# Kernel tuning notes

Measured on AMD Instinct MI355X. Metric: run time of the kernel, lower is better.

The kernel has to match this reference:

```python
import jax, jax.numpy as jnp
import numpy as np

B, T, L, H = 512, 512, 64, 512  # batch, time_steps, sequence_len, hidden_dim


def gru_cell(x, h, W_ih, W_hh, b_ih, b_hh):
    # PyTorch GRUCell math. W_ih: [3H, in], W_hh: [3H, H]; gate order (r, z, n).
    gi = x @ W_ih.T + b_ih
    gh = h @ W_hh.T + b_hh
    i_r, i_z, i_n = jnp.split(gi, 3, axis=-1)
    h_r, h_z, h_n = jnp.split(gh, 3, axis=-1)
    r = jax.nn.sigmoid(i_r + h_r)
    z = jax.nn.sigmoid(i_z + h_z)
    n = jnp.tanh(i_n + r * h_n)
    return (1.0 - z) * n + z * h


def setup_inputs() -> dict:
    key = jax.random.key(0)
    ks = jax.random.split(key, 12)
    s = 1.0 / np.sqrt(H)  # PyTorch GRUCell/Linear init scale
    u = lambda k, shape: jax.random.uniform(k, shape, jnp.float32, -s, s)
    return {
        "x": jax.random.normal(ks[0], (B, T + L - 1), jnp.float32),
        "h_1": jnp.zeros((B, H), jnp.float32),
        "h_2": jnp.zeros((B, H), jnp.float32),
        "W_ih1": u(ks[1], (3 * H, T)),
        "W_hh1": u(ks[2], (3 * H, H)),
        "b_ih1": u(ks[3], (3 * H,)),
        "b_hh1": u(ks[4], (3 * H,)),
        "W_ih2": u(ks[5], (3 * H, H)),
        "W_hh2": u(ks[6], (3 * H, H)),
        "b_ih2": u(ks[7], (3 * H,)),
        "b_hh2": u(ks[8], (3 * H,)),
        "W_fc": u(ks[9], (1, H)),
        "b_fc": u(ks[10], (1,)),
    }


def reference(x, h_1, h_2, W_ih1, W_hh1, b_ih1, b_hh1,
              W_ih2, W_hh2, b_ih2, b_hh2, W_fc, b_fc):
    # Sliding windows x[:, t:t+T] for t in [0, L): gather once, scan over steps.
    idx = jnp.arange(L)[:, None] + jnp.arange(T)[None, :]  # [L, T]
    xs = jnp.transpose(x[:, idx], (1, 0, 2))  # [L, B, T]

    def step(carry, x_t):
        h1, h2 = carry
        h1 = gru_cell(x_t, h1, W_ih1, W_hh1, b_ih1, b_hh1)
        h2 = gru_cell(h1, h2, W_ih2, W_hh2, b_ih2, b_hh2)
        y = (h2 @ W_fc.T + b_fc)[:, 0]  # [B]
        return (h1, h2), y

    (h1, h2), ys = jax.lax.scan(step, (h_1, h_2), xs)
    return ys.T, h1, h2  # output_seq [B, L], final hidden states
```

## Files before the change

### kernel.cpp

```cpp
#include <hip/hip_runtime.h>
#include <hip/hip_bf16.h>
#include <math.h>

typedef __attribute__((ext_vector_type(8))) short short8;
typedef __attribute__((ext_vector_type(4))) float f32x4;
typedef unsigned short u16;
typedef unsigned int u32;

__device__ __forceinline__ u16 f2bf(float f) {
  union { float f; u32 u; } x; x.f = f;
  return (u16)((x.u + 0x7fffu + ((x.u >> 16) & 1u)) >> 16);
}
__device__ __forceinline__ float sigm(float v) {
  return __builtin_amdgcn_rcpf(1.0f + __expf(-v));
}
__device__ __forceinline__ float tanh_fast(float v) {
  return 1.0f - 2.0f * __builtin_amdgcn_rcpf(1.0f + __expf(2.0f * v));
}

#define MFMA __builtin_amdgcn_mfma_f32_16x16x32_bf16
#define HS 262144

#define LDG16_BODY(FL)                                        \
    "global_load_dwordx4 %0, %16, off " FL "\n\t"             \
    "global_load_dwordx4 %1, %16, off offset:64 " FL "\n\t"   \
    "global_load_dwordx4 %2, %16, off offset:128 " FL "\n\t"  \
    "global_load_dwordx4 %3, %16, off offset:192 " FL "\n\t"  \
    "global_load_dwordx4 %4, %16, off offset:256 " FL "\n\t"  \
    "global_load_dwordx4 %5, %16, off offset:320 " FL "\n\t"  \
    "global_load_dwordx4 %6, %16, off offset:384 " FL "\n\t"  \
    "global_load_dwordx4 %7, %16, off offset:448 " FL "\n\t"  \
    "global_load_dwordx4 %8, %16, off offset:512 " FL "\n\t"  \
    "global_load_dwordx4 %9, %16, off offset:576 " FL "\n\t"  \
    "global_load_dwordx4 %10, %16, off offset:640 " FL "\n\t" \
    "global_load_dwordx4 %11, %16, off offset:704 " FL "\n\t" \
    "global_load_dwordx4 %12, %16, off offset:768 " FL "\n\t" \
    "global_load_dwordx4 %13, %16, off offset:832 " FL "\n\t" \
    "global_load_dwordx4 %14, %16, off offset:896 " FL "\n\t" \
    "global_load_dwordx4 %15, %16, off offset:960 " FL
#define LDG16_OPS(a, base)                                                     \
    : "=&v"(a[0]), "=&v"(a[1]), "=&v"(a[2]), "=&v"(a[3]), "=&v"(a[4]),         \
      "=&v"(a[5]), "=&v"(a[6]), "=&v"(a[7]), "=&v"(a[8]), "=&v"(a[9]),         \
      "=&v"(a[10]), "=&v"(a[11]), "=&v"(a[12]), "=&v"(a[13]), "=&v"(a[14]),    \
      "=&v"(a[15])                                                             \
    : "v"(base) : "memory"

__device__ __forceinline__ void ldg16nw_sc0(short8 a[16], const u16* base) {
  asm volatile(LDG16_BODY("sc0") LDG16_OPS(a, base));
}
__device__ __forceinline__ void ldg16nw_sc01(short8 a[16], const u16* base) {
  asm volatile(LDG16_BODY("sc0 sc1") LDG16_OPS(a, base));
}
#define VMCNT16() do { asm volatile("s_waitcnt vmcnt(16)" ::: "memory"); \
                       __builtin_amdgcn_sched_barrier(0); } while (0)
#define VMCNT0()  do { asm volatile("s_waitcnt vmcnt(0)"  ::: "memory"); \
                       __builtin_amdgcn_sched_barrier(0); } while (0)

__device__ __forceinline__ void stg_sc01(u32* p, u32 v) {
  asm volatile("global_store_dword %0, %1, off sc0 sc1" :: "v"(p), "v"(v) : "memory");
}

__device__ __forceinline__ void waits_nf(unsigned* a, unsigned ta, unsigned* b, unsigned tb) {
  if (threadIdx.x == 0) {
    while (__hip_atomic_load(a, __ATOMIC_RELAXED, __HIP_MEMORY_SCOPE_AGENT) < ta)
      __builtin_amdgcn_s_sleep(1);
    while (__hip_atomic_load(b, __ATOMIC_RELAXED, __HIP_MEMORY_SCOPE_AGENT) < tb)
      __builtin_amdgcn_s_sleep(1);
  }
  __syncthreads();
}

__device__ __forceinline__ float ydot(const short8 a[16], const float* wfcl, int quad) {
  float y = 0.0f;
  #pragma unroll
  for (int s = 0; s < 16; ++s) {
    const float4 wa = *(const float4*)&wfcl[32 * s + quad * 8];
    const float4 wb = *(const float4*)&wfcl[32 * s + quad * 8 + 4];
    union { short8 v; u32 u4[4]; } aa; aa.v = a[s];
    #pragma unroll
    for (int k = 0; k < 4; ++k) {
      union { u32 u; float f; } lo, hi;
      lo.u = aa.u4[k] << 16;
      hi.u = aa.u4[k] & 0xffff0000u;
      float w0 = (k < 2) ? ((k & 1) ? wa.z : wa.x) : ((k & 1) ? wb.z : wb.x);
      float w1 = (k < 2) ? ((k & 1) ? wa.w : wa.y) : ((k & 1) ? wb.w : wb.y);
      y = fmaf(lo.f, w0, y);
      y = fmaf(hi.f, w1, y);
    }
  }
  return y;
}

__global__ __launch_bounds__(256, 1) void gru_fused(
    const float* __restrict__ xin, const float* __restrict__ h1in, const float* __restrict__ h2in,
    const float* __restrict__ Wih1, const float* __restrict__ Whh1,
    const float* __restrict__ bih1, const float* __restrict__ bhh1,
    const float* __restrict__ Wih2, const float* __restrict__ Whh2,
    const float* __restrict__ bih2, const float* __restrict__ bhh2,
    const float* __restrict__ Wfc, const float* __restrict__ bfc,
    float* __restrict__ out, u16* __restrict__ wsb, unsigned* __restrict__ barc)
{
  const int bid   = blockIdx.x;
  const int rb    = bid & 3;
  const int layer = (bid >> 2) & 1;
  const int cbl   = bid >> 3;
  const int n0    = cbl * 16;
  const int wid   = bid >> 2;
  const int tid   = threadIdx.x;
  const int w     = tid >> 6;
  const int lane  = tid & 63;
  const int quad  = lane >> 4;
  const int m16   = lane & 15;

  u16* x0  = wsb;
  u16* x1  = x0 + 512 * 576;
  u16* h1r = x1 + 512 * 576;
  u16* h2r = h1r + 4 * HS;
  u16* h1m = h2r + 4 * HS;

  __shared__ short8 wlds[96 * 64];
  __shared__ float wfcl[512];

  unsigned* c0    = barc + rb * 32;
  unsigned* c1    = barc + 256 + rb * 32;
  unsigned* cinit = barc + 512;

  const float* Wih = layer ? Wih2 : Wih1;
  const float* Whh = layer ? Whh2 : Whh1;
  const float* bih = layer ? bih2 : bih1;
  const float* bhh = layer ? bhh2 : bhh1;

  for (int i = wid * 256 + tid; i < 128 * 575; i += 64 * 256) {
    int r = i / 575, c = i - r * 575;
    int row = rb * 128 + r;
    u16 bv = f2bf(xin[row * 575 + c]);
    x0[row * 576 + c] = bv;
    if (c >= 1) x1[row * 576 + (c - 1)] = bv;
  }
  for (int i = wid * 256 + tid; i < 128 * 512; i += 64 * 256) {
    int r = i >> 9, c = i & 511;
    int row = rb * 128 + r;
    u16 h1v = f2bf(h1in[row * 512 + c]);
    h1r[3 * HS + row * 512 + c] = h1v;
    h2r[3 * HS + row * 512 + c] = f2bf(h2in[row * 512 + c]);
  }
  for (int i = tid; i < 96 * 64; i += 256) {
    int blk = i >> 6, l = i & 63;
    int s, gr;
    if (blk < 64) { s = blk & 31; gr = (blk >> 5) * 512; }
    else          { s = blk - 64; gr = 1024; }
    int n  = n0 + (l & 15);
    int k0 = s * 32 + (l >> 4) * 8;
    short8 pk;
    #pragma unroll
    for (int j = 0; j < 8; ++j) {
      int k = k0 + j;
      float v = (k < 512) ? Wih[(gr + n) * 512 + k] : Whh[(gr + n) * 512 + (k - 512)];
      pk[j] = (short)f2bf(v);
    }
    wlds[blk * 64 + l] = pk;
  }
  for (int i = tid; i < 512; i += 256) wfcl[i] = Wfc[i];

  float hreg[2][4];
  const float* hin = layer ? h2in : h1in;
  #pragma unroll
  for (int rf = 0; rf < 2; ++rf)
    #pragma unroll
    for (int q = 0; q < 4; ++q)
      hreg[rf][q] = hin[(rb * 128 + (2 * w + rf) * 16 + quad * 4 + q) * 512 + n0 + m16];

  const int nn = n0 + m16;
  const float bias_r  = bih[nn] + bhh[nn];
  const float bias_z  = bih[512 + nn] + bhh[512 + nn];
  const float bias_in = bih[1024 + nn];
  const float bias_hn = bhh[1024 + nn];
  const float bfcv = bfc[0];

  __syncthreads();
  if (tid == 0) {
    __builtin_amdgcn_fence(__ATOMIC_RELEASE, "agent");
    __hip_atomic_fetch_add(cinit, 1u, __ATOMIC_RELAXED, __HIP_MEMORY_SCOPE_AGENT);
    while (__hip_atomic_load(cinit, __ATOMIC_RELAXED, __HIP_MEMORY_SCOPE_AGENT) < 256u)
      __builtin_amdgcn_s_sleep(1);
    __builtin_amdgcn_fence(__ATOMIC_ACQUIRE, "agent");
  }
  __syncthreads();

  const int arow0 = rb * 128 + (2 * w) * 16 + m16;
  const int arow1 = arow0 + 16;

  if (layer == 0) {
    for (int u = 0; u < 64; ++u) {
      f32x4 acc[2][4] = {};
      {
        const int c = u & 1;
        const u16* xc = c ? x1 : x0;
        const u32* pa0 = (const u32*)(xc + (size_t)arow0 * 576 + (u - c) + quad * 8);
        const u32* pa1 = (const u32*)(xc + (size_t)arow1 * 576 + (u - c) + quad * 8);
        #pragma unroll
        for (int s = 0; s < 16; ++s) {
          union { short8 v; u32 u4[4]; } a0, a1;
          #pragma unroll
          for (int j = 0; j < 4; ++j) { a0.u4[j] = pa0[s * 16 + j]; a1.u4[j] = pa1[s * 16 + j]; }
          short8 br = wlds[(s)      * 64 + lane];
          short8 bz = wlds[(32 + s) * 64 + lane];
          short8 bi = wlds[(64 + s) * 64 + lane];
          acc[0][0] = MFMA(a0.v, br, acc[0][0], 0, 0, 0);
          acc[1][0] = MFMA(a1.v, br, acc[1][0], 0, 0, 0);
          acc[0][1] = MFMA(a0.v, bz, acc[0][1], 0, 0, 0);
          acc[1][1] = MFMA(a1.v, bz, acc[1][1], 0, 0, 0);
          acc[0][2] = MFMA(a0.v, bi, acc[0][2], 0, 0, 0);
          acc[1][2] = MFMA(a1.v, bi, acc[1][2], 0, 0, 0);
        }
      }
      waits_nf(c0, 32u * (unsigned)u, c1, u >= 4 ? 32u * (unsigned)(u - 3) : 0u);
      {
        short8 a0[16], a1[16];
        const u16* hb = h1r + (size_t)((u + 3) & 3) * HS + quad * 8;
        ldg16nw_sc0(a0, hb + (size_t)arow0 * 512);
        ldg16nw_sc0(a1, hb + (size_t)arow1 * 512);
        VMCNT16();
        #pragma unroll
        for (int s = 0; s < 16; ++s) {
          short8 br = wlds[(16 + s) * 64 + lane];
          short8 bz = wlds[(48 + s) * 64 + lane];
          short8 bh = wlds[(80 + s) * 64 + lane];
          acc[0][0] = MFMA(a0[s], br, acc[0][0], 0, 0, 0);
          acc[0][1] = MFMA(a0[s], bz, acc[0][1], 0, 0, 0);
          acc[0][3] = MFMA(a0[s], bh, acc[0][3], 0, 0, 0);
        }
        VMCNT0();
        #pragma unroll
        for (int s = 0; s < 16; ++s) {
          short8 br = wlds[(16 + s) * 64 + lane];
          short8 bz = wlds[(48 + s) * 64 + lane];
          short8 bh = wlds[(80 + s) * 64 + lane];
          acc[1][0] = MFMA(a1[s], br, acc[1][0], 0, 0, 0);
          acc[1][1] = MFMA(a1[s], bz, acc[1][1], 0, 0, 0);
          acc[1][3] = MFMA(a1[s], bh, acc[1][3], 0, 0, 0);
        }
      }
      {
        u32* hw32 = (u32*)(h1r + (size_t)(u & 3) * HS);
        u32* hm   = (u32*)(h1m + (size_t)(u & 3) * HS);
        #pragma unroll
        for (int rf = 0; rf < 2; ++rf)
          #pragma unroll
          for (int q = 0; q < 4; ++q) {
            float rg = sigm(acc[rf][0][q] + bias_r);
            float zg = sigm(acc[rf][1][q] + bias_z);
            float ng = tanh_fast(acc[rf][2][q] + bias_in + rg * (acc[rf][3][q] + bias_hn));
            float hv = (1.0f - zg) * ng + zg * hreg[rf][q];
            hreg[rf][q] = hv;
            int row = rb * 128 + (2 * w + rf) * 16 + quad * 4 + q;
            u16 b = f2bf(hv);
            int pb = __shfl_xor((int)(u32)b, 1);
            if (!(m16 & 1)) {
              u32 pr = (u32)b | ((u32)(u16)pb << 16);
              int pi = (row * 512 + nn) >> 1;
              hw32[pi] = pr;
              stg_sc01(&hm[pi], pr);
            }
          }
      }
      asm volatile("s_waitcnt vmcnt(0)" ::: "memory");
      __syncthreads();
      if (tid == 0)
        __hip_atomic_fetch_add(c0, 1u, __ATOMIC_RELAXED, __HIP_MEMORY_SCOPE_AGENT);
    }
  } else {
    const bool ywg = (cbl == 0);
    for (int v = 0; v < 64; ++v) {
      f32x4 acc[2][4] = {};
      waits_nf(c1, 32u * (unsigned)v, c0, 32u * (unsigned)(v + 1));
      float ya0 = 0.0f, ya1 = 0.0f;
      {
        short8 a0[16], a1[16];
        const u16* hb = h2r + (size_t)((v + 3) & 3) * HS + quad * 8;
        ldg16nw_sc0(a0, hb + (size_t)arow0 * 512);
        ldg16nw_sc0(a1, hb + (size_t)arow1 * 512);
        VMCNT16();
        #pragma unroll
        for (int s = 0; s < 16; ++s) {
          short8 br = wlds[(16 + s) * 64 + lane];
          short8 bz = wlds[(48 + s) * 64 + lane];
          short8 bh = wlds[(80 + s) * 64 + lane];
          acc[0][0] = MFMA(a0[s], br, acc[0][0], 0, 0, 0);
          acc[0][1] = MFMA(a0[s], bz, acc[0][1], 0, 0, 0);
          acc[0][3] = MFMA(a0[s], bh, acc[0][3], 0, 0, 0);
        }
        if (ywg && v > 0) ya0 = ydot(a0, wfcl, quad);
        VMCNT0();
        #pragma unroll
        for (int s = 0; s < 16; ++s) {
          short8 br = wlds[(16 + s) * 64 + lane];
          short8 bz = wlds[(48 + s) * 64 + lane];
          short8 bh = wlds[(80 + s) * 64 + lane];
          acc[1][0] = MFMA(a1[s], br, acc[1][0], 0, 0, 0);
          acc[1][1] = MFMA(a1[s], bz, acc[1][1], 0, 0, 0);
          acc[1][3] = MFMA(a1[s], bh, acc[1][3], 0, 0, 0);
        }
        if (ywg && v > 0) ya1 = ydot(a1, wfcl, quad);
      }
      {
        short8 b0[16], b1[16];
        const u16* hb = h1m + (size_t)(v & 3) * HS + quad * 8;
        ldg16nw_sc01(b0, hb + (size_t)arow0 * 512);
        ldg16nw_sc01(b1, hb + (size_t)arow1 * 512);
        VMCNT16();
        #pragma unroll
        for (int s = 0; s < 16; ++s) {
          short8 br = wlds[(s)      * 64 + lane];
          short8 bz = wlds[(32 + s) * 64 + lane];
          short8 bi = wlds[(64 + s) * 64 + lane];
          acc[0][0] = MFMA(b0[s], br, acc[0][0], 0, 0, 0);
          acc[0][1] = MFMA(b0[s], bz, acc[0][1], 0, 0, 0);
          acc[0][2] = MFMA(b0[s], bi, acc[0][2], 0, 0, 0);
        }
        VMCNT0();
        #pragma unroll
        for (int s = 0; s < 16; ++s) {
          short8 br = wlds[(s)      * 64 + lane];
          short8 bz = wlds[(32 + s) * 64 + lane];
          short8 bi = wlds[(64 + s) * 64 + lane];
          acc[1][0] = MFMA(b1[s], br, acc[1][0], 0, 0, 0);
          acc[1][1] = MFMA(b1[s], bz, acc[1][1], 0, 0, 0);
          acc[1][2] = MFMA(b1[s], bi, acc[1][2], 0, 0, 0);
        }
      }
      {
        u32* hw32 = (u32*)(h2r + (size_t)(v & 3) * HS);
        #pragma unroll
        for (int rf = 0; rf < 2; ++rf)
          #pragma unroll
          for (int q = 0; q < 4; ++q) {
            float rg = sigm(acc[rf][0][q] + bias_r);
            float zg = sigm(acc[rf][1][q] + bias_z);
            float ng = tanh_fast(acc[rf][2][q] + bias_in + rg * (acc[rf][3][q] + bias_hn));
            float hv = (1.0f - zg) * ng + zg * hreg[rf][q];
            hreg[rf][q] = hv;
            int row = rb * 128 + (2 * w + rf) * 16 + quad * 4 + q;
            u16 b = f2bf(hv);
            int pb = __shfl_xor((int)(u32)b, 1);
            if (!(m16 & 1))
              hw32[(row * 512 + nn) >> 1] = (u32)b | ((u32)(u16)pb << 16);
          }
      }
      asm volatile("s_waitcnt vmcnt(0)" ::: "memory");
      __syncthreads();
      if (tid == 0)
        __hip_atomic_fetch_add(c1, 1u, __ATOMIC_RELAXED, __HIP_MEMORY_SCOPE_AGENT);
      if (ywg && v > 0) {
        ya0 += __shfl_xor(ya0, 16); ya0 += __shfl_xor(ya0, 32);
        ya1 += __shfl_xor(ya1, 16); ya1 += __shfl_xor(ya1, 32);
        if (quad == 0) {
          out[arow0 * 64 + (v - 1)] = ya0 + bfcv;
          out[arow1 * 64 + (v - 1)] = ya1 + bfcv;
        }
      }
    }
    if (ywg) {
      waits_nf(c1, 32u * 64u, c1, 32u * 64u);
      short8 a0[16], a1[16];
      const u16* hb = h2r + (size_t)3 * HS + quad * 8;
      ldg16nw_sc0(a0, hb + (size_t)arow0 * 512);
      ldg16nw_sc0(a1, hb + (size_t)arow1 * 512);
      VMCNT16();
      float ya0 = ydot(a0, wfcl, quad);
      VMCNT0();
      float ya1 = ydot(a1, wfcl, quad);
      ya0 += __shfl_xor(ya0, 16); ya0 += __shfl_xor(ya0, 32);
      ya1 += __shfl_xor(ya1, 16); ya1 += __shfl_xor(ya1, 32);
      if (quad == 0) {
        out[arow0 * 64 + 63] = ya0 + bfcv;
        out[arow1 * 64 + 63] = ya1 + bfcv;
      }
    }
  }

  float* hout = out + 32768 + layer * (512 * 512);
  #pragma unroll
  for (int rf = 0; rf < 2; ++rf)
    #pragma unroll
    for (int q = 0; q < 4; ++q) {
      int row = rb * 128 + (2 * w + rf) * 16 + quad * 4 + q;
      hout[row * 512 + nn] = hreg[rf][q];
    }
}

extern "C" void kernel_launch(void* const* d_in, const int* in_sizes, int n_in,
                              void* d_out, int out_size, void* d_ws, size_t ws_size,
                              hipStream_t stream) {
  (void)in_sizes; (void)n_in; (void)out_size; (void)ws_size;
  hipMemsetAsync(d_out, 0, 32768 * sizeof(float), stream);
  hipMemsetAsync(d_ws, 0, 4096, stream);
  unsigned* bar = (unsigned*)d_ws;
  u16* wsb = (u16*)((char*)d_ws + 4096);
  gru_fused<<<256, 256, 0, stream>>>(
      (const float*)d_in[0], (const float*)d_in[1], (const float*)d_in[2],
      (const float*)d_in[3], (const float*)d_in[4], (const float*)d_in[5], (const float*)d_in[6],
      (const float*)d_in[7], (const float*)d_in[8], (const float*)d_in[9], (const float*)d_in[10],
      (const float*)d_in[11], (const float*)d_in[12],
      (float*)d_out, wsb, bar);
}
```

Baseline: 801.9 us.

## Use eight pre-shifted bf16 x copies for aligned vector loads, shrink h ring buffers

The input sequence is now stored as eight column-shifted bf16 copies. Each sliding-window A operand for layer 0 can then be fetched with aligned 16-byte global_load_dwordx4 instructions instead of many scalar u32 loads. The h1r/h2r recurrence buffers drop from four slots to two, and h1m's slot 3 is seeded with the initial h1. The split VMCNT16/VMCNT0 waits that overlapped the second half of each load with the first half of the MFMAs are replaced by a single full wait, with the MFMAs for both row groups interleaved. This trades a larger prologue copy and less load/compute overlap for fewer, wider loads and a smaller working set.

```diff
diff --git a/kernel.cpp b/kernel.cpp
--- a/kernel.cpp
+++ b/kernel.cpp
@@ -20,6 +20,7 @@
 
 #define MFMA __builtin_amdgcn_mfma_f32_16x16x32_bf16
 #define HS 262144
+#define XS (512*576)
 
 #define LDG16_BODY(FL)                                        \
     "global_load_dwordx4 %0, %16, off " FL "\n\t"             \
@@ -45,15 +46,18 @@
       "=&v"(a[15])                                                             \
     : "v"(base) : "memory"
 
+__device__ __forceinline__ void ldg16nw(short8 a[16], const u16* base) {
+  asm volatile(LDG16_BODY("") LDG16_OPS(a, base));
+}
 __device__ __forceinline__ void ldg16nw_sc0(short8 a[16], const u16* base) {
   asm volatile(LDG16_BODY("sc0") LDG16_OPS(a, base));
 }
 __device__ __forceinline__ void ldg16nw_sc01(short8 a[16], const u16* base) {
   asm volatile(LDG16_BODY("sc0 sc1") LDG16_OPS(a, base));
 }
+#define VMCNT0()  do { asm volatile("s_waitcnt vmcnt(0)"  ::: "memory"); \
+                       __builtin_amdgcn_sched_barrier(0); } while (0)
 #define VMCNT16() do { asm volatile("s_waitcnt vmcnt(16)" ::: "memory"); \
-                       __builtin_amdgcn_sched_barrier(0); } while (0)
-#define VMCNT0()  do { asm volatile("s_waitcnt vmcnt(0)"  ::: "memory"); \
                        __builtin_amdgcn_sched_barrier(0); } while (0)
 
 __device__ __forceinline__ void stg_sc01(u32* p, u32 v) {
@@ -112,11 +116,10 @@
   const int quad  = lane >> 4;
   const int m16   = lane & 15;
 
-  u16* x0  = wsb;
-  u16* x1  = x0 + 512 * 576;
-  u16* h1r = x1 + 512 * 576;
-  u16* h2r = h1r + 4 * HS;
-  u16* h1m = h2r + 4 * HS;
+  u16* xc8 = wsb;
+  u16* h1r = xc8 + 8 * XS;
+  u16* h2r = h1r + 2 * HS;
+  u16* h1m = h2r + 2 * HS;
 
   __shared__ short8 wlds[96 * 64];
   __shared__ float wfcl[512];
@@ -134,15 +137,17 @@
     int r = i / 575, c = i - r * 575;
     int row = rb * 128 + r;
     u16 bv = f2bf(xin[row * 575 + c]);
-    x0[row * 576 + c] = bv;
-    if (c >= 1) x1[row * 576 + (c - 1)] = bv;
+    #pragma unroll
+    for (int k = 0; k < 8; ++k)
+      if (c >= k) xc8[k * XS + row * 576 + (c - k)] = bv;
   }
   for (int i = wid * 256 + tid; i < 128 * 512; i += 64 * 256) {
     int r = i >> 9, c = i & 511;
     int row = rb * 128 + r;
     u16 h1v = f2bf(h1in[row * 512 + c]);
-    h1r[3 * HS + row * 512 + c] = h1v;
-    h2r[3 * HS + row * 512 + c] = f2bf(h2in[row * 512 + c]);
+    h1r[1 * HS + row * 512 + c] = h1v;
+    h2r[1 * HS + row * 512 + c] = f2bf(h2in[row * 512 + c]);
+    h1m[3 * HS + row * 512 + c] = h1v;
   }
   for (int i = tid; i < 96 * 64; i += 256) {
     int blk = i >> 6, l = i & 63;
@@ -194,55 +199,46 @@
     for (int u = 0; u < 64; ++u) {
       f32x4 acc[2][4] = {};
       {
-        const int c = u & 1;
-        const u16* xc = c ? x1 : x0;
-        const u32* pa0 = (const u32*)(xc + (size_t)arow0 * 576 + (u - c) + quad * 8);
-        const u32* pa1 = (const u32*)(xc + (size_t)arow1 * 576 + (u - c) + quad * 8);
+        short8 xa0[16], xa1[16];
+        const u16* xb = xc8 + (size_t)(u & 7) * XS + (u - (u & 7)) + quad * 8;
+        ldg16nw(xa0, xb + (size_t)arow0 * 576);
+        ldg16nw(xa1, xb + (size_t)arow1 * 576);
+        VMCNT0();
         #pragma unroll
         for (int s = 0; s < 16; ++s) {
-          union { short8 v; u32 u4[4]; } a0, a1;
-          #pragma unroll
-          for (int j = 0; j < 4; ++j) { a0.u4[j] = pa0[s * 16 + j]; a1.u4[j] = pa1[s * 16 + j]; }
           short8 br = wlds[(s)      * 64 + lane];
           short8 bz = wlds[(32 + s) * 64 + lane];
           short8 bi = wlds[(64 + s) * 64 + lane];
-          acc[0][0] = MFMA(a0.v, br, acc[0][0], 0, 0, 0);
-          acc[1][0] = MFMA(a1.v, br, acc[1][0], 0, 0, 0);
-          acc[0][1] = MFMA(a0.v, bz, acc[0][1], 0, 0, 0);
-          acc[1][1] = MFMA(a1.v, bz, acc[1][1], 0, 0, 0);
-          acc[0][2] = MFMA(a0.v, bi, acc[0][2], 0, 0, 0);
-          acc[1][2] = MFMA(a1.v, bi, acc[1][2], 0, 0, 0);
+          acc[0][0] = MFMA(xa0[s], br, acc[0][0], 0, 0, 0);
+          acc[1][0] = MFMA(xa1[s], br, acc[1][0], 0, 0, 0);
+          acc[0][1] = MFMA(xa0[s], bz, acc[0][1], 0, 0, 0);
+          acc[1][1] = MFMA(xa1[s], bz, acc[1][1], 0, 0, 0);
+          acc[0][2] = MFMA(xa0[s], bi, acc[0][2], 0, 0, 0);
+          acc[1][2] = MFMA(xa1[s], bi, acc[1][2], 0, 0, 0);
         }
       }
       waits_nf(c0, 32u * (unsigned)u, c1, u >= 4 ? 32u * (unsigned)(u - 3) : 0u);
       {
         short8 a0[16], a1[16];
-        const u16* hb = h1r + (size_t)((u + 3) & 3) * HS + quad * 8;
+        const u16* hb = h1r + (size_t)((u + 1) & 1) * HS + quad * 8;
         ldg16nw_sc0(a0, hb + (size_t)arow0 * 512);
         ldg16nw_sc0(a1, hb + (size_t)arow1 * 512);
-        VMCNT16();
+        VMCNT0();
         #pragma unroll
         for (int s = 0; s < 16; ++s) {
           short8 br = wlds[(16 + s) * 64 + lane];
           short8 bz = wlds[(48 + s) * 64 + lane];
           short8 bh = wlds[(80 + s) * 64 + lane];
           acc[0][0] = MFMA(a0[s], br, acc[0][0], 0, 0, 0);
+          acc[1][0] = MFMA(a1[s], br, acc[1][0], 0, 0, 0);
           acc[0][1] = MFMA(a0[s], bz, acc[0][1], 0, 0, 0);
+          acc[1][1] = MFMA(a1[s], bz, acc[1][1], 0, 0, 0);
           acc[0][3] = MFMA(a0[s], bh, acc[0][3], 0, 0, 0);
-        }
-        VMCNT0();
-        #pragma unroll
-        for (int s = 0; s < 16; ++s) {
-          short8 br = wlds[(16 + s) * 64 + lane];
-          short8 bz = wlds[(48 + s) * 64 + lane];
-          short8 bh = wlds[(80 + s) * 64 + lane];
-          acc[1][0] = MFMA(a1[s], br, acc[1][0], 0, 0, 0);
-          acc[1][1] = MFMA(a1[s], bz, acc[1][1], 0, 0, 0);
           acc[1][3] = MFMA(a1[s], bh, acc[1][3], 0, 0, 0);
         }
       }
       {
-        u32* hw32 = (u32*)(h1r + (size_t)(u & 3) * HS);
+        u32* hw32 = (u32*)(h1r + (size_t)(u & 1) * HS);
         u32* hm   = (u32*)(h1m + (size_t)(u & 3) * HS);
         #pragma unroll
         for (int rf = 0; rf < 2; ++rf)
@@ -277,60 +273,45 @@
       float ya0 = 0.0f, ya1 = 0.0f;
       {
         short8 a0[16], a1[16];
-        const u16* hb = h2r + (size_t)((v + 3) & 3) * HS + quad * 8;
+        const u16* hb = h2r + (size_t)((v + 1) & 1) * HS + quad * 8;
         ldg16nw_sc0(a0, hb + (size_t)arow0 * 512);
         ldg16nw_sc0(a1, hb + (size_t)arow1 * 512);
-        VMCNT16();
+        VMCNT0();
         #pragma unroll
         for (int s = 0; s < 16; ++s) {
           short8 br = wlds[(16 + s) * 64 + lane];
           short8 bz = wlds[(48 + s) * 64 + lane];
           short8 bh = wlds[(80 + s) * 64 + lane];
           acc[0][0] = MFMA(a0[s], br, acc[0][0], 0, 0, 0);
+          acc[1][0] = MFMA(a1[s], br, acc[1][0], 0, 0, 0);
           acc[0][1] = MFMA(a0[s], bz, acc[0][1], 0, 0, 0);
+          acc[1][1] = MFMA(a1[s], bz, acc[1][1], 0, 0, 0);
           acc[0][3] = MFMA(a0[s], bh, acc[0][3], 0, 0, 0);
-        }
-        if (ywg && v > 0) ya0 = ydot(a0, wfcl, quad);
-        VMCNT0();
-        #pragma unroll
-        for (int s = 0; s < 16; ++s) {
-          short8 br = wlds[(16 + s) * 64 + lane];
-          short8 bz = wlds[(48 + s) * 64 + lane];
-          short8 bh = wlds[(80 + s) * 64 + lane];
-          acc[1][0] = MFMA(a1[s], br, acc[1][0], 0, 0, 0);
-          acc[1][1] = MFMA(a1[s], bz, acc[1][1], 0, 0, 0);
           acc[1][3] = MFMA(a1[s], bh, acc[1][3], 0, 0, 0);
         }
-        if (ywg && v > 0) ya1 = ydot(a1, wfcl, quad);
+        if (ywg && v > 0) { ya0 = ydot(a0, wfcl, quad); ya1 = ydot(a1, wfcl, quad); }
       }
       {
         short8 b0[16], b1[16];
         const u16* hb = h1m + (size_t)(v & 3) * HS + quad * 8;
         ldg16nw_sc01(b0, hb + (size_t)arow0 * 512);
         ldg16nw_sc01(b1, hb + (size_t)arow1 * 512);
-        VMCNT16();
+        VMCNT0();
         #pragma unroll
         for (int s = 0; s < 16; ++s) {
           short8 br = wlds[(s)      * 64 + lane];
           short8 bz = wlds[(32 + s) * 64 + lane];
           short8 bi = wlds[(64 + s) * 64 + lane];
           acc[0][0] = MFMA(b0[s], br, acc[0][0], 0, 0, 0);
+          acc[1][0] = MFMA(b1[s], br, acc[1][0], 0, 0, 0);
           acc[0][1] = MFMA(b0[s], bz, acc[0][1], 0, 0, 0);
+          acc[1][1] = MFMA(b1[s], bz, acc[1][1], 0, 0, 0);
           acc[0][2] = MFMA(b0[s], bi, acc[0][2], 0, 0, 0);
-        }
-        VMCNT0();
-        #pragma unroll
-        for (int s = 0; s < 16; ++s) {
-          short8 br = wlds[(s)      * 64 + lane];
-          short8 bz = wlds[(32 + s) * 64 + lane];
-          short8 bi = wlds[(64 + s) * 64 + lane];
-          acc[1][0] = MFMA(b1[s], br, acc[1][0], 0, 0, 0);
-          acc[1][1] = MFMA(b1[s], bz, acc[1][1], 0, 0, 0);
           acc[1][2] = MFMA(b1[s], bi, acc[1][2], 0, 0, 0);
         }
       }
       {
-        u32* hw32 = (u32*)(h2r + (size_t)(v & 3) * HS);
+        u32* hw32 = (u32*)(h2r + (size_t)(v & 1) * HS);
         #pragma unroll
         for (int rf = 0; rf < 2; ++rf)
           #pragma unroll
@@ -363,7 +344,7 @@
     if (ywg) {
       waits_nf(c1, 32u * 64u, c1, 32u * 64u);
       short8 a0[16], a1[16];
-      const u16* hb = h2r + (size_t)3 * HS + quad * 8;
+      const u16* hb = h2r + (size_t)1 * HS + quad * 8;
       ldg16nw_sc0(a0, hb + (size_t)arow0 * 512);
       ldg16nw_sc0(a1, hb + (size_t)arow1 * 512);
       VMCNT16();
```

After: 819.7 us. +2.2%, slower.
